# Performance work log

Measured on AMD Instinct MI355X. Metric: run time of the kernel, lower is better.

## Reference

```python
import jax, jax.numpy as jnp
import numpy as np

GROUPS = 6  # attn_group in Stack

def setup_inputs() -> dict:
    key = jax.random.key(0)
    k0, k1, k2, k3, k4 = jax.random.split(key, 5)
    B, S, IN, OUT, K = 2, 2048, 512, 768, 31
    fan = (2.0 / IN) ** 0.5  # kaiming_normal fan_out-ish scale
    x = jax.random.normal(k0, (B, S, IN), jnp.float32)
    W_q = jax.random.normal(k1, (OUT, IN), jnp.float32) * fan
    W_k = jax.random.normal(k2, (OUT, IN), jnp.float32) * fan
    W_v = jax.random.normal(k3, (OUT, IN), jnp.float32) * fan
    rel = jax.random.normal(k4, (OUT, K), jnp.float32)
    return {"x": x, "W_q": W_q, "W_k": W_k, "W_v": W_v, "rel": rel}

def reference(x, W_q, W_k, W_v, rel):
    B, S, _ = x.shape
    OUT, K = rel.shape
    pad = (K - 1) // 2
    d = OUT // GROUPS
    # projections
    q = x @ W_q.T                                   # [B,S,OUT]
    xp = jnp.pad(x, ((0, 0), (pad, pad), (0, 0)))    # pad seq dim
    k = xp @ W_k.T                                  # [B,S+K-1,OUT]
    v = xp @ W_v.T
    # unfold: window of size K per query position (stride 1)
    idx = jnp.arange(S)[:, None] + jnp.arange(K)[None, :]   # [S,K]
    k_win = k[:, idx, :] + rel.T                    # [B,S,K,OUT], rel bias (out,K)->(K,out)
    v_win = v[:, idx, :]                            # [B,S,K,OUT]
    k_win = k_win.reshape(B, S, K, GROUPS, d)
    v_win = v_win.reshape(B, S, K, GROUPS, d)
    qg = q.reshape(B, S, GROUPS, d)
    energy = jnp.einsum('bsgd,bskgd->bsgk', qg, k_win)       # QK dot over head dim
    attn = jax.nn.softmax(energy, axis=-1)                   # softmax over window
    out = jnp.einsum('bsgk,bskgd->bsgd', attn, v_win).reshape(B, S, OUT)
    return out, attn  # attn matches torch attention.squeeze(3): [B,S,groups,K]
```

## Files before the change

kernel.cpp:

```cpp
#include <hip/hip_runtime.h>
#include <hip/hip_bf16.h>

#define S_LEN 2048
#define B_SZ 2
#define IN_DIM 512
#define OUT_DIM 768
#define KWIN 31
#define PAD 15
#define NGROUP 6
#define DHEAD 128
#define M_TOT 4096
#define N_TOT 2304
#define QK_W 1536

typedef __attribute__((ext_vector_type(8))) __bf16 bf16x8;
typedef __attribute__((ext_vector_type(8))) unsigned short u16x8;
typedef __attribute__((ext_vector_type(4))) float f32x4;

static __device__ __forceinline__ unsigned short f2bf(float f) {
  unsigned int u = __float_as_uint(f);
  unsigned int r = (u + 0x7fffu + ((u >> 16) & 1u)) >> 16;
  return (unsigned short)r;
}
static __device__ __forceinline__ float bf2f(unsigned short h) {
  return __uint_as_float(((unsigned int)h) << 16);
}

__global__ __launch_bounds__(256) void prep_kernel(
    const float* __restrict__ x,
    const float* __restrict__ Wq, const float* __restrict__ Wk, const float* __restrict__ Wv,
    const float* __restrict__ rel,
    unsigned short* __restrict__ xhi, unsigned short* __restrict__ xlo,
    unsigned short* __restrict__ whi, unsigned short* __restrict__ wlo,
    unsigned short* __restrict__ relThi, unsigned short* __restrict__ relTlo,
    unsigned short* __restrict__ zpage) {
  const int bid = blockIdx.x;
  const int tid = threadIdx.x;
  if (bid < 2048) {
    int i = bid * 256 + tid;
    float4 v = ((const float4*)x)[i];
    unsigned short h0 = f2bf(v.x), h1 = f2bf(v.y), h2 = f2bf(v.z), h3 = f2bf(v.w);
    ((ushort4*)xhi)[i] = make_ushort4(h0, h1, h2, h3);
    ((ushort4*)xlo)[i] = make_ushort4(f2bf(v.x - bf2f(h0)), f2bf(v.y - bf2f(h1)),
                                      f2bf(v.z - bf2f(h2)), f2bf(v.w - bf2f(h3)));
  } else if (bid < 3200) {
    int i = (bid - 2048) * 256 + tid;
    int e = i * 4;
    const int per = OUT_DIM * IN_DIM;
    const float* src = (e < per) ? Wq : (e < 2 * per) ? Wk : Wv;
    int rem = (e < per) ? e : (e < 2 * per) ? e - per : e - 2 * per;
    float4 v = *(const float4*)(src + rem);
    unsigned short h0 = f2bf(v.x), h1 = f2bf(v.y), h2 = f2bf(v.z), h3 = f2bf(v.w);
    ((ushort4*)whi)[i] = make_ushort4(h0, h1, h2, h3);
    ((ushort4*)wlo)[i] = make_ushort4(f2bf(v.x - bf2f(h0)), f2bf(v.y - bf2f(h1)),
                                      f2bf(v.z - bf2f(h2)), f2bf(v.w - bf2f(h3)));
  } else if (bid < 3293) {
    int idx = (bid - 3200) * 256 + tid;
    int kk = idx / OUT_DIM;
    int o = idx - kk * OUT_DIM;
    float v = rel[o * KWIN + kk];
    unsigned short h = f2bf(v);
    relThi[idx] = h;
    relTlo[idx] = f2bf(v - bf2f(h));
  } else {
    if (tid < 128) zpage[tid] = 0;
  }
}

#define SLOTB 49152

static __device__ __forceinline__ int swz32(int O) {
  return O ^ (((O >> 7) & 3) << 4);
}

#define MFMA16(AF, BF) \
  _Pragma("unroll") for (int mi = 0; mi < 4; ++mi) \
  _Pragma("unroll") for (int ni = 0; ni < 4; ++ni) \
    acc[mi][ni] = __builtin_amdgcn_mfma_f32_16x16x32_bf16( \
        AF[mi], BF[ni], acc[mi][ni], 0, 0, 0);

#define READ_AHI() _Pragma("unroll") for (int mi = 0; mi < 4; ++mi) ahi[mi] = *(const bf16x8*)(slot + aoff[mi]);
#define READ_ALO() _Pragma("unroll") for (int mi = 0; mi < 4; ++mi) alo[mi] = *(const bf16x8*)(slot + 16384 + aoff[mi]);
#define READ_WHI() _Pragma("unroll") for (int ni = 0; ni < 4; ++ni) whi[ni] = *(const bf16x8*)(slot + 32768 + boff[ni]);
#define READ_WLO() _Pragma("unroll") for (int ni = 0; ni < 4; ++ni) wlo[ni] = *(const bf16x8*)(slot + 40960 + boff[ni]);

#define END_BARRIER() \
  __builtin_amdgcn_s_barrier(); \
  asm volatile("" ::: "memory");

__global__ __launch_bounds__(512, 2) void gemm_kernel(
    const unsigned short* __restrict__ Ahi, const unsigned short* __restrict__ Alo,
    const unsigned short* __restrict__ Whi, const unsigned short* __restrict__ Wlo,
    unsigned short* __restrict__ qkhi, unsigned short* __restrict__ qklo,
    unsigned short* __restrict__ vTw) {
  __shared__ unsigned short lds_u16[73728];
  char* ldsb = (char*)lds_u16;
  const int tid = threadIdx.x;
  const int wid = tid >> 6, lane = tid & 63;
  const int elr = lane & 15, elq = lane >> 4;
  const int wm = wid >> 1, wn = wid & 1;

  int aoff[4], boff[4];
#pragma unroll
  for (int mi = 0; mi < 4; ++mi)
    aoff[mi] = swz32((wm * 64 + mi * 16 + elr) * 64 + elq * 16);
#pragma unroll
  for (int ni = 0; ni < 4; ++ni)
    boff[ni] = swz32((wn * 64 + ni * 16 + elr) * 64 + elq * 16);

  const int strow = tid >> 2;
  const int stcol = (((tid & 3) ^ ((tid >> 3) & 3)) << 3);

  auto stage8k = [&](char* slot, int RO, int j, const unsigned short* src,
                     int grow0, int kloc) {
    const unsigned short* g = src + (size_t)(grow0 + j * 128 + strow) * IN_DIM + kloc + stcol;
    __builtin_amdgcn_global_load_lds((const __attribute__((address_space(1))) void*)g,
        (__attribute__((address_space(3))) void*)(slot + RO + j * 8192 + wid * 1024), 16, 0, 0);
  };

  f32x4 acc[4][4] = {};
  bf16x8 ahi[4], whi[4], alo[4], wlo[4];

  const int bid = blockIdx.x;

  if (bid < 192) {
    const int bm = bid & 15, ct = bid >> 4;
    const int row0 = bm << 8, col0 = ct << 7;

    auto stageChunk = [&](int cc) {
      char* s = ldsb + (cc % 3) * SLOTB;
      const int pk = cc << 5;
      stage8k(s, 0, 0, Ahi, row0, pk);      stage8k(s, 0, 1, Ahi, row0, pk);
      stage8k(s, 16384, 0, Alo, row0, pk);  stage8k(s, 16384, 1, Alo, row0, pk);
      stage8k(s, 32768, 0, Whi, col0, pk);  stage8k(s, 40960, 0, Wlo, col0, pk);
    };

    stageChunk(0);
    stageChunk(1);
    asm volatile("s_waitcnt vmcnt(6)" ::: "memory");
    END_BARRIER()

    for (int c = 0; c < 16; ++c) {
      char* slot = ldsb + (c % 3) * SLOTB;
      READ_AHI()
      READ_WHI()
      READ_ALO()
      READ_WLO()
      const bool pref = (c + 2) < 16;
      if (pref) stageChunk(c + 2);
      __builtin_amdgcn_s_setprio(1);
      MFMA16(ahi, whi)
      MFMA16(alo, whi)
      MFMA16(ahi, wlo)
      __builtin_amdgcn_s_setprio(0);
      if (pref) { asm volatile("s_waitcnt vmcnt(6)" ::: "memory"); }
      else      { asm volatile("s_waitcnt vmcnt(0)" ::: "memory"); }
      END_BARRIER()
    }

    const int elg = elq * 4;
#pragma unroll
    for (int mi = 0; mi < 4; ++mi)
#pragma unroll
      for (int ni = 0; ni < 4; ++ni) {
        int ncol = col0 + wn * 64 + ni * 16 + elr;
        size_t rbase = (size_t)(row0 + wm * 64 + mi * 16 + elg);
#pragma unroll
        for (int j = 0; j < 4; ++j) {
          float v = acc[mi][ni][j];
          unsigned short h = f2bf(v);
          size_t idx = (rbase + j) * QK_W + ncol;
          qkhi[idx] = h;
          qklo[idx] = f2bf(v - bf2f(h));
        }
      }
  } else {
    const int bid2 = bid - 192;
    const int bm = bid2 & 15, grp = bid2 >> 4;
    const int row0 = bm << 8;
    auto vcol = [&](int ci) { return 1536 + ((grp * 2 + (ci >> 4)) << 7); };

    auto stageChunkV = [&](int cc) {
      char* s = ldsb + (cc % 3) * SLOTB;
      const int pk = (cc & 15) << 5;
      stage8k(s, 0, 0, Ahi, row0, pk);  stage8k(s, 0, 1, Ahi, row0, pk);
      stage8k(s, 32768, 0, Whi, vcol(cc), pk);
    };

    stageChunkV(0);
    stageChunkV(1);
    asm volatile("s_waitcnt vmcnt(3)" ::: "memory");
    END_BARRIER()

    for (int ci = 0; ci < 32; ++ci) {
      char* slot = ldsb + (ci % 3) * SLOTB;
      READ_AHI()
      READ_WHI()
      const bool pref = (ci + 2) < 32;
      if (pref) stageChunkV(ci + 2);
      __builtin_amdgcn_s_setprio(1);
      MFMA16(ahi, whi)
      __builtin_amdgcn_s_setprio(0);
      if (pref) { asm volatile("s_waitcnt vmcnt(3)" ::: "memory"); }
      else      { asm volatile("s_waitcnt vmcnt(0)" ::: "memory"); }
      END_BARRIER()

      if ((ci & 15) == 15) {
        const int col0 = vcol(ci);
        const int elg = elq * 4;
#pragma unroll
        for (int mi = 0; mi < 4; ++mi)
#pragma unroll
          for (int ni = 0; ni < 4; ++ni) {
            int d = col0 - 1536 + wn * 64 + ni * 16 + elr;
            int srw = row0 + wm * 64 + mi * 16 + elg;
            ushort4 pk4;
            pk4.x = f2bf(acc[mi][ni][0]); pk4.y = f2bf(acc[mi][ni][1]);
            pk4.z = f2bf(acc[mi][ni][2]); pk4.w = f2bf(acc[mi][ni][3]);
            *(ushort4*)(vTw + (size_t)d * M_TOT + srw) = pk4;
            acc[mi][ni] = (f32x4){0.f, 0.f, 0.f, 0.f};
          }
      }
    }
  }
}

__global__ __launch_bounds__(256, 2) void attn_kernel(
    const unsigned short* __restrict__ qkhi, const unsigned short* __restrict__ qklo,
    const unsigned short* __restrict__ vT,
    const unsigned short* __restrict__ relThi, const unsigned short* __restrict__ relTlo,
    const unsigned short* __restrict__ zpage,
    float* __restrict__ out, float* __restrict__ attn_out) {
  __shared__ __attribute__((aligned(16))) unsigned short smem[40960];
  char* smb = (char*)smem;
  float* Elds = (float*)(smb + 69632);

  const int tid = threadIdx.x;
  const int wid = tid >> 6, lane = tid & 63;
  const int bid = blockIdx.x;
  const int tile = bid & 63;
  const int g = (bid >> 6) % NGROUP;
  const int b = bid / (64 * NGROUP);
  const int s0 = tile * 32;
  const size_t rowbase = (size_t)b * S_LEN;
  const int elr = lane & 15, elq = lane >> 4;

  {
    const int wrow = wid * 4 + (lane >> 4);
    const int kcb = lane & 15;
#pragma unroll
    for (int arr = 0; arr < 2; ++arr) {
      const unsigned short* src = arr ? qklo : qkhi;
      const unsigned short* rsrc = arr ? relTlo : relThi;
      const int ldsbase = arr ? 24576 : 0;
#pragma unroll
      for (int i = 0; i < 6; ++i) {
        int w = i * 16 + wrow;
        int scb = (kcb ^ (w & 7)) * 8;
        const unsigned short* gp;
        if (w < 62) {
          int r = s0 - 15 + w;
          gp = (r >= 0 && r < S_LEN)
             ? src + (size_t)(rowbase + r) * QK_W + OUT_DIM + g * DHEAD + scb
             : zpage + scb;
        } else if (w < 93) {
          gp = rsrc + (w - 62) * OUT_DIM + g * DHEAD + scb;
        } else {
          gp = zpage + scb;
        }
        __builtin_amdgcn_global_load_lds((const __attribute__((address_space(1))) void*)gp,
            (__attribute__((address_space(3))) void*)(smb + ldsbase + (i * 16 + wid * 4) * 256 + (lane & 15) * 16 + (lane >> 4) * 256),
            16, 0, 0);
      }
    }
  }
  {
    const unsigned short* vsrc = vT + (size_t)g * DHEAD * M_TOT + (size_t)b * S_LEN;
    const int drow = wid * 8 + (lane >> 3);
    const int vcb = lane & 7;
#pragma unroll
    for (int i = 0; i < 4; ++i) {
      int d = i * 32 + drow;
      int sl = s0 - 16 + (vcb ^ (d & 7)) * 8;
      const unsigned short* gp = (sl >= 0 && sl < S_LEN)
        ? vsrc + (size_t)d * M_TOT + sl
        : zpage + (vcb ^ (d & 7)) * 8;
      __builtin_amdgcn_global_load_lds((const __attribute__((address_space(1))) void*)gp,
          (__attribute__((address_space(3))) void*)(smb + 49152 + (i * 32 + wid * 8) * 128 + (lane >> 3) * 128 + (lane & 7) * 16),
          16, 0, 0);
    }
  }
  {
    int O = tid * 16;
    O ^= (O >> 3) & 0x70;
    u16x8 z = {};
    *(u16x8*)(smb + 65536 + O) = z;
  }

  const int rf = wid & 1;
  const int cb3 = 3 * (wid >> 1);
  bf16x8 qh[4], ql[4];
  {
    size_t qrow = rowbase + s0 + rf * 16 + elr;
    const unsigned short* qb  = qkhi + qrow * QK_W + g * DHEAD + elq * 8;
    const unsigned short* qb2 = qklo + qrow * QK_W + g * DHEAD + elq * 8;
#pragma unroll
    for (int ks = 0; ks < 4; ++ks) {
      qh[ks] = *(const bf16x8*)(qb + ks * 32);
      ql[ks] = *(const bf16x8*)(qb2 + ks * 32);
    }
  }
  __syncthreads();

#pragma unroll
  for (int cf = 0; cf < 3; ++cf) {
    int c = cb3 + cf;
    f32x4 ea = {};
#pragma unroll
    for (int ks = 0; ks < 4; ++ks) {
      int O = (c * 16 + elr) * 256 + ks * 64 + elq * 16;
      int Os = O ^ ((O >> 4) & 0x70);
      bf16x8 kh = *(const bf16x8*)(smb + Os);
      bf16x8 kl = *(const bf16x8*)(smb + 24576 + Os);
      ea = __builtin_amdgcn_mfma_f32_16x16x32_bf16(qh[ks], kh, ea, 0, 0, 0);
      ea = __builtin_amdgcn_mfma_f32_16x16x32_bf16(ql[ks], kh, ea, 0, 0, 0);
      ea = __builtin_amdgcn_mfma_f32_16x16x32_bf16(qh[ks], kl, ea, 0, 0, 0);
    }
#pragma unroll
    for (int j = 0; j < 4; ++j)
      Elds[(rf * 16 + elq * 4 + j) * 96 + c * 16 + elr] = ea[j];
  }
  __syncthreads();

  {
    const int kkl = lane & 31;
    const int half = lane >> 5;
    const int kkc = (kkl < 31) ? kkl : 30;
#pragma unroll
    for (int p = 0; p < 4; ++p) {
      int si = p * 8 + wid * 2 + half;
      float e = Elds[si * 96 + si + kkc] + Elds[si * 96 + 62 + kkc];
      if (kkl == 31) e = -INFINITY;
      float m = e;
#pragma unroll
      for (int off = 16; off > 0; off >>= 1) m = fmaxf(m, __shfl_xor(m, off, 32));
      float pr = __expf(e - m);
      float sum = pr;
#pragma unroll
      for (int off = 16; off > 0; off >>= 1) sum += __shfl_xor(sum, off, 32);
      float a = pr / sum;
      if (kkl < 31) {
        attn_out[((rowbase + s0 + si) * NGROUP + g) * KWIN + kkl] = a;
        int O = si * 128 + (si + kkl + 1) * 2;
        O ^= (O >> 3) & 0x70;
        *(unsigned short*)(smb + 65536 + O) = f2bf(a);
      }
    }
  }
  __syncthreads();

  {
    const int pcb = 4 * (wid >> 1);
    f32x4 pa[4] = {};
#pragma unroll
    for (int ks = 0; ks < 2; ++ks) {
      int AO = (rf * 16 + elr) * 128 + ks * 64 + elq * 16;
      AO ^= (AO >> 3) & 0x70;
      bf16x8 afr = *(const bf16x8*)(smb + 65536 + AO);
#pragma unroll
      for (int cf = 0; cf < 4; ++cf) {
        int VO = ((pcb + cf) * 16 + elr) * 128 + ks * 64 + elq * 16;
        VO ^= (VO >> 3) & 0x70;
        bf16x8 vfr = *(const bf16x8*)(smb + 49152 + VO);
        pa[cf] = __builtin_amdgcn_mfma_f32_16x16x32_bf16(afr, vfr, pa[cf], 0, 0, 0);
      }
    }
#pragma unroll
    for (int cf = 0; cf < 4; ++cf)
#pragma unroll
      for (int j = 0; j < 4; ++j)
        out[(rowbase + s0 + rf * 16 + elq * 4 + j) * OUT_DIM + g * DHEAD + pcb * 16 + cf * 16 + elr]
            = pa[cf][j];
  }
}

extern "C" void kernel_launch(void* const* d_in, const int* in_sizes, int n_in,
                              void* d_out, int out_size, void* d_ws, size_t ws_size,
                              hipStream_t stream) {
  const float* x   = (const float*)d_in[0];
  const float* Wq  = (const float*)d_in[1];
  const float* Wk  = (const float*)d_in[2];
  const float* Wv  = (const float*)d_in[3];
  const float* rel = (const float*)d_in[4];

  char* ws = (char*)d_ws;
  unsigned short* Ahi    = (unsigned short*)(ws);
  unsigned short* Alo    = (unsigned short*)(ws + 4194304);
  unsigned short* Whi    = (unsigned short*)(ws + 8388608);
  unsigned short* Wlo    = (unsigned short*)(ws + 10747904);
  unsigned short* relThi = (unsigned short*)(ws + 13107200);
  unsigned short* relTlo = (unsigned short*)(ws + 13154816);
  unsigned short* qkhi   = (unsigned short*)(ws + 13202432);
  unsigned short* qklo   = (unsigned short*)(ws + 25785344);
  unsigned short* vTw    = (unsigned short*)(ws + 38368256);
  unsigned short* zpage  = (unsigned short*)(ws + 44659712);

  float* outp = (float*)d_out;
  float* attn = outp + (size_t)B_SZ * S_LEN * OUT_DIM;

  prep_kernel<<<3294, 256, 0, stream>>>(x, Wq, Wk, Wv, rel, Ahi, Alo, Whi, Wlo,
                                        relThi, relTlo, zpage);
  gemm_kernel<<<240, 512, 0, stream>>>(Ahi, Alo, Whi, Wlo, qkhi, qklo, vTw);
  attn_kernel<<<768, 256, 0, stream>>>(qkhi, qklo, vTw, relThi, relTlo, zpage, outp, attn);
}
```

Baseline: 56.64 us.

## Shrink GEMM tiles to 128x128 with 256 threads and double buffering

The projection GEMM now uses 128x128 output tiles with 4 waves per block instead of 256x128 tiles with 8 waves. This doubles the grid to 480 blocks so more of the CUs get work. The LDS ring drops from three slots to two, with a prefetch depth of one chunk and a full vmcnt(0) wait every iteration. The aim is better CU occupancy and less LDS per block. The cost is more redundant loads of the weight operand and less latency hiding in the load pipeline.

```diff
diff --git a/kernel.cpp b/kernel.cpp
--- a/kernel.cpp
+++ b/kernel.cpp
@@ -67,7 +67,7 @@
   }
 }
 
-#define SLOTB 49152
+#define SLOTB 32768
 
 static __device__ __forceinline__ int swz32(int O) {
   return O ^ (((O >> 7) & 3) << 4);
@@ -80,20 +80,20 @@
         AF[mi], BF[ni], acc[mi][ni], 0, 0, 0);
 
 #define READ_AHI() _Pragma("unroll") for (int mi = 0; mi < 4; ++mi) ahi[mi] = *(const bf16x8*)(slot + aoff[mi]);
-#define READ_ALO() _Pragma("unroll") for (int mi = 0; mi < 4; ++mi) alo[mi] = *(const bf16x8*)(slot + 16384 + aoff[mi]);
-#define READ_WHI() _Pragma("unroll") for (int ni = 0; ni < 4; ++ni) whi[ni] = *(const bf16x8*)(slot + 32768 + boff[ni]);
-#define READ_WLO() _Pragma("unroll") for (int ni = 0; ni < 4; ++ni) wlo[ni] = *(const bf16x8*)(slot + 40960 + boff[ni]);
+#define READ_ALO() _Pragma("unroll") for (int mi = 0; mi < 4; ++mi) alo[mi] = *(const bf16x8*)(slot + 8192 + aoff[mi]);
+#define READ_WHI() _Pragma("unroll") for (int ni = 0; ni < 4; ++ni) whi[ni] = *(const bf16x8*)(slot + 16384 + boff[ni]);
+#define READ_WLO() _Pragma("unroll") for (int ni = 0; ni < 4; ++ni) wlo[ni] = *(const bf16x8*)(slot + 24576 + boff[ni]);
 
 #define END_BARRIER() \
   __builtin_amdgcn_s_barrier(); \
   asm volatile("" ::: "memory");
 
-__global__ __launch_bounds__(512, 2) void gemm_kernel(
+__global__ __launch_bounds__(256, 2) void gemm_kernel(
     const unsigned short* __restrict__ Ahi, const unsigned short* __restrict__ Alo,
     const unsigned short* __restrict__ Whi, const unsigned short* __restrict__ Wlo,
     unsigned short* __restrict__ qkhi, unsigned short* __restrict__ qklo,
     unsigned short* __restrict__ vTw) {
-  __shared__ unsigned short lds_u16[73728];
+  __shared__ unsigned short lds_u16[32768];
   char* ldsb = (char*)lds_u16;
   const int tid = threadIdx.x;
   const int wid = tid >> 6, lane = tid & 63;
@@ -111,11 +111,14 @@
   const int strow = tid >> 2;
   const int stcol = (((tid & 3) ^ ((tid >> 3) & 3)) << 3);
 
-  auto stage8k = [&](char* slot, int RO, int j, const unsigned short* src,
+  auto stage8k = [&](char* slot, int RO, const unsigned short* src,
                      int grow0, int kloc) {
-    const unsigned short* g = src + (size_t)(grow0 + j * 128 + strow) * IN_DIM + kloc + stcol;
-    __builtin_amdgcn_global_load_lds((const __attribute__((address_space(1))) void*)g,
-        (__attribute__((address_space(3))) void*)(slot + RO + j * 8192 + wid * 1024), 16, 0, 0);
+#pragma unroll
+    for (int j = 0; j < 2; ++j) {
+      const unsigned short* g = src + (size_t)(grow0 + j * 64 + strow) * IN_DIM + kloc + stcol;
+      __builtin_amdgcn_global_load_lds((const __attribute__((address_space(1))) void*)g,
+          (__attribute__((address_space(3))) void*)(slot + RO + j * 4096 + wid * 1024), 16, 0, 0);
+    }
   };
 
   f32x4 acc[4][4] = {};
@@ -123,38 +126,36 @@
 
   const int bid = blockIdx.x;
 
-  if (bid < 192) {
-    const int bm = bid & 15, ct = bid >> 4;
-    const int row0 = bm << 8, col0 = ct << 7;
+  if (bid < 384) {
+    const int bm = bid & 31, ct = bid >> 5;
+    const int row0 = bm << 7, col0 = ct << 7;
 
     auto stageChunk = [&](int cc) {
-      char* s = ldsb + (cc % 3) * SLOTB;
+      char* s = ldsb + (cc & 1) * SLOTB;
       const int pk = cc << 5;
-      stage8k(s, 0, 0, Ahi, row0, pk);      stage8k(s, 0, 1, Ahi, row0, pk);
-      stage8k(s, 16384, 0, Alo, row0, pk);  stage8k(s, 16384, 1, Alo, row0, pk);
-      stage8k(s, 32768, 0, Whi, col0, pk);  stage8k(s, 40960, 0, Wlo, col0, pk);
+      stage8k(s, 0, Ahi, row0, pk);
+      stage8k(s, 8192, Alo, row0, pk);
+      stage8k(s, 16384, Whi, col0, pk);
+      stage8k(s, 24576, Wlo, col0, pk);
     };
 
     stageChunk(0);
-    stageChunk(1);
-    asm volatile("s_waitcnt vmcnt(6)" ::: "memory");
+    asm volatile("s_waitcnt vmcnt(0)" ::: "memory");
     END_BARRIER()
 
     for (int c = 0; c < 16; ++c) {
-      char* slot = ldsb + (c % 3) * SLOTB;
+      char* slot = ldsb + (c & 1) * SLOTB;
       READ_AHI()
       READ_WHI()
       READ_ALO()
       READ_WLO()
-      const bool pref = (c + 2) < 16;
-      if (pref) stageChunk(c + 2);
+      if (c + 1 < 16) stageChunk(c + 1);
       __builtin_amdgcn_s_setprio(1);
       MFMA16(ahi, whi)
       MFMA16(alo, whi)
       MFMA16(ahi, wlo)
       __builtin_amdgcn_s_setprio(0);
-      if (pref) { asm volatile("s_waitcnt vmcnt(6)" ::: "memory"); }
-      else      { asm volatile("s_waitcnt vmcnt(0)" ::: "memory"); }
+      asm volatile("s_waitcnt vmcnt(0)" ::: "memory");
       END_BARRIER()
     }
 
@@ -175,34 +176,31 @@
         }
       }
   } else {
-    const int bid2 = bid - 192;
-    const int bm = bid2 & 15, grp = bid2 >> 4;
-    const int row0 = bm << 8;
+    const int bid2 = bid - 384;
+    const int bm = bid2 & 31, grp = bid2 >> 5;
+    const int row0 = bm << 7;
     auto vcol = [&](int ci) { return 1536 + ((grp * 2 + (ci >> 4)) << 7); };
 
     auto stageChunkV = [&](int cc) {
-      char* s = ldsb + (cc % 3) * SLOTB;
+      char* s = ldsb + (cc & 1) * SLOTB;
       const int pk = (cc & 15) << 5;
-      stage8k(s, 0, 0, Ahi, row0, pk);  stage8k(s, 0, 1, Ahi, row0, pk);
-      stage8k(s, 32768, 0, Whi, vcol(cc), pk);
+      stage8k(s, 0, Ahi, row0, pk);
+      stage8k(s, 16384, Whi, vcol(cc), pk);
     };
 
     stageChunkV(0);
-    stageChunkV(1);
-    asm volatile("s_waitcnt vmcnt(3)" ::: "memory");
+    asm volatile("s_waitcnt vmcnt(0)" ::: "memory");
     END_BARRIER()
 
     for (int ci = 0; ci < 32; ++ci) {
-      char* slot = ldsb + (ci % 3) * SLOTB;
+      char* slot = ldsb + (ci & 1) * SLOTB;
       READ_AHI()
       READ_WHI()
-      const bool pref = (ci + 2) < 32;
-      if (pref) stageChunkV(ci + 2);
+      if (ci + 1 < 32) stageChunkV(ci + 1);
       __builtin_amdgcn_s_setprio(1);
       MFMA16(ahi, whi)
       __builtin_amdgcn_s_setprio(0);
-      if (pref) { asm volatile("s_waitcnt vmcnt(3)" ::: "memory"); }
-      else      { asm volatile("s_waitcnt vmcnt(0)" ::: "memory"); }
+      asm volatile("s_waitcnt vmcnt(0)" ::: "memory");
       END_BARRIER()
 
       if ((ci & 15) == 15) {
@@ -410,6 +408,6 @@
 
   prep_kernel<<<3294, 256, 0, stream>>>(x, Wq, Wk, Wv, rel, Ahi, Alo, Whi, Wlo,
                                         relThi, relTlo, zpage);
-  gemm_kernel<<<240, 512, 0, stream>>>(Ahi, Alo, Whi, Wlo, qkhi, qklo, vTw);
+  gemm_kernel<<<480, 256, 0, stream>>>(Ahi, Alo, Whi, Wlo, qkhi, qklo, vTw);
   attn_kernel<<<768, 256, 0, stream>>>(qkhi, qklo, vTw, relThi, relTlo, zpage, outp, attn);
 }
```

Result: slower. 58.37 us (+3.0%).
